# Kernel optimization log

Measured on AMD Instinct MI355X. Metric: run time of the kernel, lower is better.

## Reference

```python
import jax, jax.numpy as jnp
import numpy as np

NEG_INF = -10000.0
ALPHA = 0.2      # LeakyReLU slope
EPS = 1e-5       # LayerNorm eps
B, N, D = 8, 2048, 128


def setup_inputs() -> dict:
    key = jax.random.key(0)
    ks = jax.random.split(key, 8)
    x = jax.random.normal(ks[0], (B, N, D), dtype=jnp.float32)
    adj_bool = jax.random.randint(ks[1], (B, N, N), 0, 2, dtype=jnp.int32)
    node_mask = jax.random.randint(ks[2], (B, N), 0, 2, dtype=jnp.int32)
    s = 1.0 / np.sqrt(D)
    W = jax.random.uniform(ks[3], (D, D), jnp.float32, -s, s)    # fc weight (in->out)
    a_l = jax.random.uniform(ks[4], (D,), jnp.float32, -s, s)    # attn_l weight
    a_r = jax.random.uniform(ks[5], (D,), jnp.float32, -s, s)    # attn_r weight
    gamma = jnp.ones((D,), jnp.float32)                          # LayerNorm weight
    beta = jnp.zeros((D,), jnp.float32)                          # LayerNorm bias
    return {"x": x, "adj_bool": adj_bool, "node_mask": node_mask,
            "W": W, "a_l": a_l, "a_r": a_r, "gamma": gamma, "beta": beta}


def reference(x, adj_bool, node_mask, W, a_l, a_r, gamma, beta):
    m = node_mask.astype(x.dtype)[..., None]           # [B,N,1]
    x = x * m
    h = jnp.einsum('bnd,de->bne', x, W)                # [B,N,D]
    e_l = jnp.einsum('bnd,d->bn', h, a_l)              # [B,N]
    e_r = jnp.einsum('bnd,d->bn', h, a_r)              # [B,N]
    e = e_l[:, :, None] + e_r[:, None, :]              # [B,N,N]
    e = jnp.where(e > 0, e, ALPHA * e)                 # LeakyReLU
    pair = (node_mask[:, :, None] * node_mask[:, None, :]) > 0
    allowed = (adj_bool > 0) & pair
    e = jnp.where(allowed, e, NEG_INF)
    attn = jax.nn.softmax(e, axis=-1)                  # finite (NEG_INF fill), nan_to_num is a no-op
    out = jnp.einsum('bij,bjd->bid', attn, h)          # dropout in eval mode = identity
    out = (out + x) * m                                # residual (ind==outd), then node mask
    mu = jnp.mean(out, axis=-1, keepdims=True)
    var = jnp.var(out, axis=-1, keepdims=True)
    out = (out - mu) * jax.lax.rsqrt(var + EPS) * gamma + beta
    return out
```

## Files before the change

kernel.cpp:

```cpp
#include <hip/hip_runtime.h>
#include <stdint.h>


#define BB 8
#define NN 2048
#define DD 128
#define GAT_NEG_INF -10000.0f
#define LN_EPS 1e-5f

typedef __attribute__((ext_vector_type(8))) short short8;
typedef __attribute__((ext_vector_type(4))) float f32x4;

__device__ __forceinline__ unsigned pk_bf16(float a, float b) {
    unsigned ua = __float_as_uint(a); ua += 0x7FFFu + ((ua >> 16) & 1u);
    unsigned ub = __float_as_uint(b); ub += 0x7FFFu + ((ub >> 16) & 1u);
    return (ua >> 16) | (ub & 0xFFFF0000u);
}

__global__ __launch_bounds__(256) void fc_kernel(
    const float* __restrict__ x, const int* __restrict__ mask,
    const float* __restrict__ W, const float* __restrict__ a_l,
    const float* __restrict__ a_r, unsigned short* __restrict__ hT,
    float* __restrict__ el, float* __restrict__ er)
{
    __shared__ __align__(16) float Ws[64 * DD];
    __shared__ __align__(16) float xs[32 * 68];

    const int t  = threadIdx.x;
    const int b  = blockIdx.x >> 6;
    const int it = blockIdx.x & 63;
    const int i0 = it * 32;

    const int r  = t >> 3;
    const int c  = t & 7;
    const int o0 = c * 16;

    float acc[16];
#pragma unroll
    for (int u = 0; u < 16; ++u) acc[u] = 0.f;

    for (int kt = 0; kt < 2; ++kt) {
        __syncthreads();
        const float4* W4  = (const float4*)(W + (size_t)kt * 64 * DD);
        float4*       Ws4 = (float4*)Ws;
#pragma unroll
        for (int i = 0; i < 8; ++i) Ws4[t + 256 * i] = W4[t + 256 * i];
#pragma unroll
        for (int i = 0; i < 2; ++i) {
            int idx = t + 256 * i;
            int row = idx >> 4, c4 = idx & 15;
            float4 v = *(const float4*)(x + ((size_t)(b * NN + i0 + row)) * DD
                                          + kt * 64 + c4 * 4);
            float mm = (float)mask[b * NN + i0 + row];
            v.x *= mm; v.y *= mm; v.z *= mm; v.w *= mm;
            *(float4*)(xs + row * 68 + c4 * 4) = v;
        }
        __syncthreads();

        const float4* Wsr = (const float4*)Ws;
#pragma unroll 4
        for (int k = 0; k < 64; ++k) {
            float xv = xs[r * 68 + k];
#pragma unroll
            for (int u4 = 0; u4 < 4; ++u4) {
                float4 w = Wsr[k * 32 + c * 4 + u4];
                acc[u4 * 4 + 0] += xv * w.x;
                acc[u4 * 4 + 1] += xv * w.y;
                acc[u4 * 4 + 2] += xv * w.z;
                acc[u4 * 4 + 3] += xv * w.w;
            }
        }
    }

    float sl = 0.f, sr = 0.f;
#pragma unroll
    for (int u = 0; u < 16; ++u) {
        sl += acc[u] * a_l[o0 + u];
        sr += acc[u] * a_r[o0 + u];
    }
#pragma unroll
    for (int off = 4; off; off >>= 1) {
        sl += __shfl_xor(sl, off, 8);
        sr += __shfl_xor(sr, off, 8);
    }
    if (c == 0) {
        el[b * NN + i0 + r] = sl;
        er[b * NN + i0 + r] = sr;
    }

    __syncthreads();
    float* hTs = Ws;
#pragma unroll
    for (int u = 0; u < 16; ++u) hTs[(o0 + u) * 33 + r] = acc[u];
    __syncthreads();

    {
        int d = t >> 1, half = t & 1;
        const float* src = hTs + d * 33 + half * 16;
        unsigned pk8[8];
#pragma unroll
        for (int k = 0; k < 8; ++k) pk8[k] = pk_bf16(src[2 * k], src[2 * k + 1]);
        unsigned short* dst = hT + ((size_t)(b * DD + d)) * NN + i0 + half * 16;
        *(uint4*)dst       = make_uint4(pk8[0], pk8[1], pk8[2], pk8[3]);
        *(uint4*)(dst + 8) = make_uint4(pk8[4], pk8[5], pk8[6], pk8[7]);
    }
}

__global__ __launch_bounds__(64) void attn_kernel(
    const float* __restrict__ x, const int* __restrict__ adj,
    const int* __restrict__ mask, const unsigned short* __restrict__ hT,
    const float* __restrict__ el, const float* __restrict__ er,
    const float* __restrict__ gamma, const float* __restrict__ beta,
    float* __restrict__ outp)
{
    const int lane = threadIdx.x;
    const int row  = lane & 15;
    const int grp  = lane >> 4;
    const int b    = blockIdx.x >> 7;
    const int it   = blockIdx.x & 127;
    const int i0   = it * 16;
    const int gi   = i0 + row;

    const float el_r = el[b * NN + gi];
    const int   mi   = mask[b * NN + gi];
    const int*  adj_row = adj + ((size_t)(b * NN + gi)) * NN;
    const float* er_b = er + b * NN;
    const int*   mk_b = mask + b * NN;
    const unsigned short* hT_b = hT + (size_t)b * DD * NN;

    f32x4 acc[8];
#pragma unroll
    for (int nb = 0; nb < 8; ++nb) acc[nb] = (f32x4)0.f;
    float m_run = -3.0e38f, l_run = 0.f;

    int4 pa0, pa1, pa2, pa3;
    float4 pe0, pe1, pe2, pe3;
    int4 pq0, pq1, pq2, pq3;

    auto load_meta = [&](int jt) {
        const int jb = jt * 64 + grp * 8;
        pa0 = *(const int4*)(adj_row + jb);
        pa1 = *(const int4*)(adj_row + jb + 4);
        pa2 = *(const int4*)(adj_row + jb + 32);
        pa3 = *(const int4*)(adj_row + jb + 36);
        pe0 = *(const float4*)(er_b + jb);
        pe1 = *(const float4*)(er_b + jb + 4);
        pe2 = *(const float4*)(er_b + jb + 32);
        pe3 = *(const float4*)(er_b + jb + 36);
        pq0 = *(const int4*)(mk_b + jb);
        pq1 = *(const int4*)(mk_b + jb + 4);
        pq2 = *(const int4*)(mk_b + jb + 32);
        pq3 = *(const int4*)(mk_b + jb + 36);
    };
    load_meta(0);

    union BU { int4 q; short8 v; };
    union AU { unsigned u[4]; short8 v; };

#pragma unroll 1
    for (int jt = 0; jt < NN / 64; ++jt) {
        int4 a0 = pa0, a1 = pa1, a2 = pa2, a3 = pa3;
        float4 e0 = pe0, e1 = pe1, e2 = pe2, e3 = pe3;
        int4 q0 = pq0, q1 = pq1, q2 = pq2, q3 = pq3;
        load_meta(jt < NN / 64 - 1 ? jt + 1 : jt);

        BU bf[16];
        {
            const int jb = jt * 64 + grp * 8;
#pragma unroll
            for (int s = 0; s < 2; ++s)
#pragma unroll
                for (int nb = 0; nb < 8; ++nb)
                    bf[s * 8 + nb].q = *(const int4*)(hT_b
                        + (size_t)(nb * 16 + row) * NN + jb + s * 32);
        }

        int   av[16] = {a0.x,a0.y,a0.z,a0.w, a1.x,a1.y,a1.z,a1.w,
                        a2.x,a2.y,a2.z,a2.w, a3.x,a3.y,a3.z,a3.w};
        int   qv[16] = {q0.x,q0.y,q0.z,q0.w, q1.x,q1.y,q1.z,q1.w,
                        q2.x,q2.y,q2.z,q2.w, q3.x,q3.y,q3.z,q3.w};
        float ev[16] = {e0.x,e0.y,e0.z,e0.w, e1.x,e1.y,e1.z,e1.w,
                        e2.x,e2.y,e2.z,e2.w, e3.x,e3.y,e3.z,e3.w};
        float ss[16];
        float tmax = -3.0e38f;
#pragma unroll
        for (int u = 0; u < 16; ++u) {
            float e = el_r + ev[u];
            e = fmaxf(e, 0.2f * e);
            bool ok = (av[u] & qv[u] & mi) != 0;
            ss[u] = ok ? e : GAT_NEG_INF;
            tmax = fmaxf(tmax, ss[u]);
        }
        tmax = fmaxf(tmax, __shfl_xor(tmax, 16, 64));
        tmax = fmaxf(tmax, __shfl_xor(tmax, 32, 64));
        float m_new = fmaxf(m_run, tmax);
        float al    = __expf(m_run - m_new);
        float p[16];
        float psum = 0.f;
#pragma unroll
        for (int u = 0; u < 16; ++u) {
            p[u] = __expf(ss[u] - m_new);
            psum += p[u];
        }
        psum += __shfl_xor(psum, 16, 64);
        psum += __shfl_xor(psum, 32, 64);
        l_run = l_run * al + psum;
        m_run = m_new;

        float alr[4];
#pragma unroll
        for (int reg = 0; reg < 4; ++reg) alr[reg] = __shfl(al, grp * 4 + reg, 64);
#pragma unroll
        for (int nb = 0; nb < 8; ++nb) {
            acc[nb][0] *= alr[0]; acc[nb][1] *= alr[1];
            acc[nb][2] *= alr[2]; acc[nb][3] *= alr[3];
        }

        AU A0, A1;
#pragma unroll
        for (int k = 0; k < 4; ++k) {
            A0.u[k] = pk_bf16(p[2 * k],     p[2 * k + 1]);
            A1.u[k] = pk_bf16(p[8 + 2 * k], p[8 + 2 * k + 1]);
        }

#pragma unroll
        for (int nb = 0; nb < 8; ++nb)
            acc[nb] = __builtin_amdgcn_mfma_f32_16x16x32_bf16(A0.v, bf[nb].v, acc[nb], 0, 0, 0);
#pragma unroll
        for (int nb = 0; nb < 8; ++nb)
            acc[nb] = __builtin_amdgcn_mfma_f32_16x16x32_bf16(A1.v, bf[8 + nb].v, acc[nb], 0, 0, 0);
    }

    float inv[4], mq[4];
#pragma unroll
    for (int reg = 0; reg < 4; ++reg) {
        float lq = __shfl(l_run, grp * 4 + reg, 64);
        inv[reg] = 1.0f / lq;
        mq[reg]  = (float)mk_b[i0 + grp * 4 + reg];
    }

    float v[8][4];
    float s1[4] = {0.f, 0.f, 0.f, 0.f}, s2[4] = {0.f, 0.f, 0.f, 0.f};
#pragma unroll
    for (int nb = 0; nb < 8; ++nb)
#pragma unroll
        for (int reg = 0; reg < 4; ++reg) {
            float xv = x[((size_t)(b * NN + i0 + grp * 4 + reg)) * DD + nb * 16 + row];
            float tv = (acc[nb][reg] * inv[reg] + xv) * mq[reg];
            v[nb][reg] = tv;
            s1[reg] += tv;
            s2[reg] += tv * tv;
        }
#pragma unroll
    for (int off = 1; off < 16; off <<= 1)
#pragma unroll
        for (int reg = 0; reg < 4; ++reg) {
            s1[reg] += __shfl_xor(s1[reg], off, 64);
            s2[reg] += __shfl_xor(s2[reg], off, 64);
        }

    float mu[4], rsd[4];
#pragma unroll
    for (int reg = 0; reg < 4; ++reg) {
        mu[reg] = s1[reg] * (1.0f / DD);
        float var = s2[reg] * (1.0f / DD) - mu[reg] * mu[reg];
        rsd[reg] = rsqrtf(var + LN_EPS);
    }
#pragma unroll
    for (int nb = 0; nb < 8; ++nb) {
        float g  = gamma[nb * 16 + row];
        float be = beta[nb * 16 + row];
#pragma unroll
        for (int reg = 0; reg < 4; ++reg) {
            float o = (v[nb][reg] - mu[reg]) * rsd[reg] * g + be;
            outp[((size_t)(b * NN + i0 + grp * 4 + reg)) * DD + nb * 16 + row] = o;
        }
    }
}

extern "C" void kernel_launch(void* const* d_in, const int* in_sizes, int n_in,
                              void* d_out, int out_size, void* d_ws, size_t ws_size,
                              hipStream_t stream) {
    const float* x     = (const float*)d_in[0];
    const int*   adj   = (const int*)d_in[1];
    const int*   maskp = (const int*)d_in[2];
    const float* W     = (const float*)d_in[3];
    const float* a_l   = (const float*)d_in[4];
    const float* a_r   = (const float*)d_in[5];
    const float* gamma = (const float*)d_in[6];
    const float* beta  = (const float*)d_in[7];
    float*       outp  = (float*)d_out;

    unsigned short* hT = (unsigned short*)d_ws;
    float* el = (float*)(hT + (size_t)BB * DD * NN);
    float* er = el + (size_t)BB * NN;

    fc_kernel<<<BB * (NN / 32), 256, 0, stream>>>(x, maskp, W, a_l, a_r, hT, el, er);
    attn_kernel<<<BB * (NN / 16), 64, 0, stream>>>(x, adj, maskp, hT, el, er,
                                                   gamma, beta, outp);
}
```

Measured before the change: 272.6 us.

## Split attention key range across four waves and move FC to split-bf16 MFMA

The attention kernel now runs four waves per 16-row block, each covering a quarter of the key range with its own online softmax. The partial max, sum and accumulator are merged through shared memory before the residual and LayerNorm, which are rewritten with one row per wave. This is meant to raise parallelism and occupancy for the adjacency-bandwidth-bound loop. The FC projection is rewritten to use bf16 MFMA with a hi/lo split of x and W (three products) in place of fp32 FMA, using a new prep kernel that transposes and splits W. The extra launch and merge step add some overhead, and the split-bf16 products are slightly less exact than fp32.

```diff
diff --git a/kernel.cpp b/kernel.cpp
--- a/kernel.cpp
+++ b/kernel.cpp
@@ -16,116 +16,139 @@
     unsigned ub = __float_as_uint(b); ub += 0x7FFFu + ((ub >> 16) & 1u);
     return (ua >> 16) | (ub & 0xFFFF0000u);
 }
+__device__ __forceinline__ unsigned short bf16_rtn(float a) {
+    unsigned ua = __float_as_uint(a);
+    return (unsigned short)((ua + 0x7FFFu + ((ua >> 16) & 1u)) >> 16);
+}
+
+__global__ void prep_wt(const float* __restrict__ W,
+                        unsigned short* __restrict__ WThi,
+                        unsigned short* __restrict__ WTlo)
+{
+    int idx = blockIdx.x * 256 + threadIdx.x;
+    int k = idx >> 7, n = idx & 127;
+    float w = W[idx];
+    unsigned short hi = bf16_rtn(w);
+    float hif = __uint_as_float((unsigned)hi << 16);
+    WThi[n * DD + k] = hi;
+    WTlo[n * DD + k] = bf16_rtn(w - hif);
+}
 
 __global__ __launch_bounds__(256) void fc_kernel(
     const float* __restrict__ x, const int* __restrict__ mask,
-    const float* __restrict__ W, const float* __restrict__ a_l,
-    const float* __restrict__ a_r, unsigned short* __restrict__ hT,
-    float* __restrict__ el, float* __restrict__ er)
+    const unsigned short* __restrict__ WThi, const unsigned short* __restrict__ WTlo,
+    const float* __restrict__ a_l, const float* __restrict__ a_r,
+    unsigned short* __restrict__ hT, float* __restrict__ el, float* __restrict__ er)
 {
-    __shared__ __align__(16) float Ws[64 * DD];
-    __shared__ __align__(16) float xs[32 * 68];
-
-    const int t  = threadIdx.x;
-    const int b  = blockIdx.x >> 6;
-    const int it = blockIdx.x & 63;
-    const int i0 = it * 32;
-
-    const int r  = t >> 3;
-    const int c  = t & 7;
-    const int o0 = c * 16;
-
-    float acc[16];
-#pragma unroll
-    for (int u = 0; u < 16; ++u) acc[u] = 0.f;
-
-    for (int kt = 0; kt < 2; ++kt) {
-        __syncthreads();
-        const float4* W4  = (const float4*)(W + (size_t)kt * 64 * DD);
-        float4*       Ws4 = (float4*)Ws;
-#pragma unroll
-        for (int i = 0; i < 8; ++i) Ws4[t + 256 * i] = W4[t + 256 * i];
-#pragma unroll
-        for (int i = 0; i < 2; ++i) {
-            int idx = t + 256 * i;
-            int row = idx >> 4, c4 = idx & 15;
-            float4 v = *(const float4*)(x + ((size_t)(b * NN + i0 + row)) * DD
-                                          + kt * 64 + c4 * 4);
-            float mm = (float)mask[b * NN + i0 + row];
-            v.x *= mm; v.y *= mm; v.z *= mm; v.w *= mm;
-            *(float4*)(xs + row * 68 + c4 * 4) = v;
-        }
-        __syncthreads();
-
-        const float4* Wsr = (const float4*)Ws;
-#pragma unroll 4
-        for (int k = 0; k < 64; ++k) {
-            float xv = xs[r * 68 + k];
-#pragma unroll
-            for (int u4 = 0; u4 < 4; ++u4) {
-                float4 w = Wsr[k * 32 + c * 4 + u4];
-                acc[u4 * 4 + 0] += xv * w.x;
-                acc[u4 * 4 + 1] += xv * w.y;
-                acc[u4 * 4 + 2] += xv * w.z;
-                acc[u4 * 4 + 3] += xv * w.w;
-            }
-        }
-    }
-
-    float sl = 0.f, sr = 0.f;
-#pragma unroll
-    for (int u = 0; u < 16; ++u) {
-        sl += acc[u] * a_l[o0 + u];
-        sr += acc[u] * a_r[o0 + u];
-    }
-#pragma unroll
-    for (int off = 4; off; off >>= 1) {
-        sl += __shfl_xor(sl, off, 8);
-        sr += __shfl_xor(sr, off, 8);
-    }
-    if (c == 0) {
-        el[b * NN + i0 + r] = sl;
-        er[b * NN + i0 + r] = sr;
-    }
-
-    __syncthreads();
-    float* hTs = Ws;
-#pragma unroll
-    for (int u = 0; u < 16; ++u) hTs[(o0 + u) * 33 + r] = acc[u];
-    __syncthreads();
-
-    {
-        int d = t >> 1, half = t & 1;
-        const float* src = hTs + d * 33 + half * 16;
-        unsigned pk8[8];
-#pragma unroll
-        for (int k = 0; k < 8; ++k) pk8[k] = pk_bf16(src[2 * k], src[2 * k + 1]);
-        unsigned short* dst = hT + ((size_t)(b * DD + d)) * NN + i0 + half * 16;
-        *(uint4*)dst       = make_uint4(pk8[0], pk8[1], pk8[2], pk8[3]);
-        *(uint4*)(dst + 8) = make_uint4(pk8[4], pk8[5], pk8[6], pk8[7]);
-    }
-}
-
-__global__ __launch_bounds__(64) void attn_kernel(
+    const int t    = threadIdx.x;
+    const int wv   = t >> 6;
+    const int lane = t & 63;
+    const int col  = lane & 15;
+    const int grp  = lane >> 4;
+    const int b    = blockIdx.x & 7;
+    const int it   = blockIdx.x >> 3;
+    const int i0   = it * 64 + wv * 16;
+
+    const float* xrow = x + ((size_t)(b * NN + i0 + col)) * DD + grp * 8;
+    const float  mm   = (float)mask[b * NN + i0 + col];
+
+    f32x4 acc[8];
+#pragma unroll
+    for (int nb = 0; nb < 8; ++nb) acc[nb] = (f32x4)0.f;
+
+    union AU { unsigned u[4]; short8 v; };
+    union BU { int4 q; short8 v; };
+
+#pragma unroll
+    for (int ks = 0; ks < 4; ++ks) {
+        float4 xa = *(const float4*)(xrow + ks * 32);
+        float4 xb = *(const float4*)(xrow + ks * 32 + 4);
+        float xv[8] = {xa.x, xa.y, xa.z, xa.w, xb.x, xb.y, xb.z, xb.w};
+        unsigned short hi[8]; float lo[8];
+#pragma unroll
+        for (int u = 0; u < 8; ++u) {
+            float v = xv[u] * mm;
+            hi[u] = bf16_rtn(v);
+            lo[u] = v - __uint_as_float((unsigned)hi[u] << 16);
+        }
+        AU Ahi, Alo;
+#pragma unroll
+        for (int j = 0; j < 4; ++j) {
+            Ahi.u[j] = (unsigned)hi[2 * j] | ((unsigned)hi[2 * j + 1] << 16);
+            Alo.u[j] = pk_bf16(lo[2 * j], lo[2 * j + 1]);
+        }
+#pragma unroll
+        for (int nb = 0; nb < 8; ++nb) {
+            BU Bhi, Blo;
+            Bhi.q = *(const int4*)(WThi + (nb * 16 + col) * DD + ks * 32 + grp * 8);
+            Blo.q = *(const int4*)(WTlo + (nb * 16 + col) * DD + ks * 32 + grp * 8);
+            acc[nb] = __builtin_amdgcn_mfma_f32_16x16x32_bf16(Ahi.v, Bhi.v, acc[nb], 0, 0, 0);
+            acc[nb] = __builtin_amdgcn_mfma_f32_16x16x32_bf16(Alo.v, Bhi.v, acc[nb], 0, 0, 0);
+            acc[nb] = __builtin_amdgcn_mfma_f32_16x16x32_bf16(Ahi.v, Blo.v, acc[nb], 0, 0, 0);
+        }
+    }
+
+    float sl[4] = {0.f, 0.f, 0.f, 0.f}, sr[4] = {0.f, 0.f, 0.f, 0.f};
+#pragma unroll
+    for (int nb = 0; nb < 8; ++nb) {
+        float alv = a_l[nb * 16 + col];
+        float arv = a_r[nb * 16 + col];
+#pragma unroll
+        for (int reg = 0; reg < 4; ++reg) {
+            sl[reg] += acc[nb][reg] * alv;
+            sr[reg] += acc[nb][reg] * arv;
+        }
+    }
+#pragma unroll
+    for (int off = 1; off < 16; off <<= 1)
+#pragma unroll
+        for (int reg = 0; reg < 4; ++reg) {
+            sl[reg] += __shfl_xor(sl[reg], off, 64);
+            sr[reg] += __shfl_xor(sr[reg], off, 64);
+        }
+    if (col == 0) {
+#pragma unroll
+        for (int reg = 0; reg < 4; ++reg) {
+            el[b * NN + i0 + grp * 4 + reg] = sl[reg];
+            er[b * NN + i0 + grp * 4 + reg] = sr[reg];
+        }
+    }
+
+#pragma unroll
+    for (int nb = 0; nb < 8; ++nb) {
+        unsigned p01 = pk_bf16(acc[nb][0], acc[nb][1]);
+        unsigned p23 = pk_bf16(acc[nb][2], acc[nb][3]);
+        *(uint2*)(hT + ((size_t)(b * DD + nb * 16 + col)) * NN + i0 + grp * 4) =
+            make_uint2(p01, p23);
+    }
+}
+
+__global__ __launch_bounds__(256, 4) void attn_kernel(
     const float* __restrict__ x, const int* __restrict__ adj,
     const int* __restrict__ mask, const unsigned short* __restrict__ hT,
     const float* __restrict__ el, const float* __restrict__ er,
     const float* __restrict__ gamma, const float* __restrict__ beta,
     float* __restrict__ outp)
 {
-    const int lane = threadIdx.x;
+    __shared__ __align__(16) float macc[4][16][132];
+    __shared__ float mls[4][16][2];
+
+    const int t    = threadIdx.x;
+    const int wv   = t >> 6;
+    const int lane = t & 63;
     const int row  = lane & 15;
     const int grp  = lane >> 4;
-    const int b    = blockIdx.x >> 7;
-    const int it   = blockIdx.x & 127;
+    const int b    = blockIdx.x & 7;
+    const int it   = blockIdx.x >> 3;
     const int i0   = it * 16;
     const int gi   = i0 + row;
+    const int j0   = wv * 512;
 
     const float el_r = el[b * NN + gi];
     const int   mi   = mask[b * NN + gi];
-    const int*  adj_row = adj + ((size_t)(b * NN + gi)) * NN;
-    const float* er_b = er + b * NN;
-    const int*   mk_b = mask + b * NN;
+    const int*  adj_row = adj + ((size_t)(b * NN + gi)) * NN + j0;
+    const float* er_w = er + b * NN + j0;
+    const int*   mk_w = mask + b * NN + j0;
     const unsigned short* hT_b = hT + (size_t)b * DD * NN;
 
     f32x4 acc[8];
@@ -143,14 +166,14 @@
         pa1 = *(const int4*)(adj_row + jb + 4);
         pa2 = *(const int4*)(adj_row + jb + 32);
         pa3 = *(const int4*)(adj_row + jb + 36);
-        pe0 = *(const float4*)(er_b + jb);
-        pe1 = *(const float4*)(er_b + jb + 4);
-        pe2 = *(const float4*)(er_b + jb + 32);
-        pe3 = *(const float4*)(er_b + jb + 36);
-        pq0 = *(const int4*)(mk_b + jb);
-        pq1 = *(const int4*)(mk_b + jb + 4);
-        pq2 = *(const int4*)(mk_b + jb + 32);
-        pq3 = *(const int4*)(mk_b + jb + 36);
+        pe0 = *(const float4*)(er_w + jb);
+        pe1 = *(const float4*)(er_w + jb + 4);
+        pe2 = *(const float4*)(er_w + jb + 32);
+        pe3 = *(const float4*)(er_w + jb + 36);
+        pq0 = *(const int4*)(mk_w + jb);
+        pq1 = *(const int4*)(mk_w + jb + 4);
+        pq2 = *(const int4*)(mk_w + jb + 32);
+        pq3 = *(const int4*)(mk_w + jb + 36);
     };
     load_meta(0);
 
@@ -158,15 +181,15 @@
     union AU { unsigned u[4]; short8 v; };
 
 #pragma unroll 1
-    for (int jt = 0; jt < NN / 64; ++jt) {
+    for (int jt = 0; jt < 8; ++jt) {
         int4 a0 = pa0, a1 = pa1, a2 = pa2, a3 = pa3;
         float4 e0 = pe0, e1 = pe1, e2 = pe2, e3 = pe3;
         int4 q0 = pq0, q1 = pq1, q2 = pq2, q3 = pq3;
-        load_meta(jt < NN / 64 - 1 ? jt + 1 : jt);
+        load_meta(jt < 7 ? jt + 1 : jt);
 
         BU bf[16];
         {
-            const int jb = jt * 64 + grp * 8;
+            const int jb = j0 + jt * 64 + grp * 8;
 #pragma unroll
             for (int s = 0; s < 2; ++s)
 #pragma unroll
@@ -222,7 +245,6 @@
             A0.u[k] = pk_bf16(p[2 * k],     p[2 * k + 1]);
             A1.u[k] = pk_bf16(p[8 + 2 * k], p[8 + 2 * k + 1]);
         }
-
 #pragma unroll
         for (int nb = 0; nb < 8; ++nb)
             acc[nb] = __builtin_amdgcn_mfma_f32_16x16x32_bf16(A0.v, bf[nb].v, acc[nb], 0, 0, 0);
@@ -231,50 +253,50 @@
             acc[nb] = __builtin_amdgcn_mfma_f32_16x16x32_bf16(A1.v, bf[8 + nb].v, acc[nb], 0, 0, 0);
     }
 
-    float inv[4], mq[4];
-#pragma unroll
-    for (int reg = 0; reg < 4; ++reg) {
-        float lq = __shfl(l_run, grp * 4 + reg, 64);
-        inv[reg] = 1.0f / lq;
-        mq[reg]  = (float)mk_b[i0 + grp * 4 + reg];
-    }
-
-    float v[8][4];
-    float s1[4] = {0.f, 0.f, 0.f, 0.f}, s2[4] = {0.f, 0.f, 0.f, 0.f};
+    if (grp == 0) { mls[wv][row][0] = m_run; mls[wv][row][1] = l_run; }
 #pragma unroll
     for (int nb = 0; nb < 8; ++nb)
 #pragma unroll
-        for (int reg = 0; reg < 4; ++reg) {
-            float xv = x[((size_t)(b * NN + i0 + grp * 4 + reg)) * DD + nb * 16 + row];
-            float tv = (acc[nb][reg] * inv[reg] + xv) * mq[reg];
-            v[nb][reg] = tv;
-            s1[reg] += tv;
-            s2[reg] += tv * tv;
-        }
-#pragma unroll
-    for (int off = 1; off < 16; off <<= 1)
-#pragma unroll
-        for (int reg = 0; reg < 4; ++reg) {
-            s1[reg] += __shfl_xor(s1[reg], off, 64);
-            s2[reg] += __shfl_xor(s2[reg], off, 64);
-        }
-
-    float mu[4], rsd[4];
-#pragma unroll
-    for (int reg = 0; reg < 4; ++reg) {
-        mu[reg] = s1[reg] * (1.0f / DD);
-        float var = s2[reg] * (1.0f / DD) - mu[reg] * mu[reg];
-        rsd[reg] = rsqrtf(var + LN_EPS);
-    }
-#pragma unroll
-    for (int nb = 0; nb < 8; ++nb) {
-        float g  = gamma[nb * 16 + row];
-        float be = beta[nb * 16 + row];
-#pragma unroll
-        for (int reg = 0; reg < 4; ++reg) {
-            float o = (v[nb][reg] - mu[reg]) * rsd[reg] * g + be;
-            outp[((size_t)(b * NN + i0 + grp * 4 + reg)) * DD + nb * 16 + row] = o;
-        }
+        for (int reg = 0; reg < 4; ++reg)
+            macc[wv][grp * 4 + reg][nb * 16 + row] = acc[nb][reg];
+    __syncthreads();
+
+    const float g0  = gamma[2 * lane], g1 = gamma[2 * lane + 1];
+    const float be0 = beta[2 * lane],  be1 = beta[2 * lane + 1];
+#pragma unroll
+    for (int q = 0; q < 4; ++q) {
+        const int r  = wv * 4 + q;
+        const int gir = i0 + r;
+        float m0 = mls[0][r][0], m1 = mls[1][r][0], m2 = mls[2][r][0], m3 = mls[3][r][0];
+        float m_f = fmaxf(fmaxf(m0, m1), fmaxf(m2, m3));
+        float sc0 = __expf(m0 - m_f), sc1 = __expf(m1 - m_f);
+        float sc2 = __expf(m2 - m_f), sc3 = __expf(m3 - m_f);
+        float l_f = mls[0][r][1] * sc0 + mls[1][r][1] * sc1
+                  + mls[2][r][1] * sc2 + mls[3][r][1] * sc3;
+        float inv = 1.0f / l_f;
+        float2 v0 = *(const float2*)&macc[0][r][2 * lane];
+        float2 v1 = *(const float2*)&macc[1][r][2 * lane];
+        float2 v2 = *(const float2*)&macc[2][r][2 * lane];
+        float2 v3 = *(const float2*)&macc[3][r][2 * lane];
+        float ox = v0.x * sc0 + v1.x * sc1 + v2.x * sc2 + v3.x * sc3;
+        float oy = v0.y * sc0 + v1.y * sc1 + v2.y * sc2 + v3.y * sc3;
+
+        float mq = (float)mask[b * NN + gir];
+        float2 xv = *(const float2*)(x + ((size_t)(b * NN + gir)) * DD + 2 * lane);
+        float w0 = (ox * inv + xv.x) * mq;
+        float w1 = (oy * inv + xv.y) * mq;
+
+        float s1 = w0 + w1, s2 = w0 * w0 + w1 * w1;
+#pragma unroll
+        for (int off = 32; off; off >>= 1) {
+            s1 += __shfl_xor(s1, off, 64);
+            s2 += __shfl_xor(s2, off, 64);
+        }
+        float mu  = s1 * (1.0f / DD);
+        float var = s2 * (1.0f / DD) - mu * mu;
+        float rsd = rsqrtf(var + LN_EPS);
+        *(float2*)(outp + ((size_t)(b * NN + gir)) * DD + 2 * lane) =
+            make_float2((w0 - mu) * rsd * g0 + be0, (w1 - mu) * rsd * g1 + be1);
     }
 }
 
@@ -294,8 +316,12 @@
     unsigned short* hT = (unsigned short*)d_ws;
     float* el = (float*)(hT + (size_t)BB * DD * NN);
     float* er = el + (size_t)BB * NN;
-
-    fc_kernel<<<BB * (NN / 32), 256, 0, stream>>>(x, maskp, W, a_l, a_r, hT, el, er);
-    attn_kernel<<<BB * (NN / 16), 64, 0, stream>>>(x, adj, maskp, hT, el, er,
-                                                   gamma, beta, outp);
-}
+    unsigned short* WThi = (unsigned short*)(er + (size_t)BB * NN);
+    unsigned short* WTlo = WThi + DD * DD;
+
+    prep_wt<<<64, 256, 0, stream>>>(W, WThi, WTlo);
+    fc_kernel<<<BB * (NN / 64), 256, 0, stream>>>(x, maskp, WThi, WTlo,
+                                                  a_l, a_r, hT, el, er);
+    attn_kernel<<<BB * (NN / 16), 256, 0, stream>>>(x, adj, maskp, hT, el, er,
+                                                    gamma, beta, outp);
+}
```

New measurement: 280.3 us. 2.8% more time.
